# Kernel tuning notes

Measured on AMD Instinct MI355X. Metric: run time of the kernel, lower is better.

Reference implementation:

```python
import jax, jax.numpy as jnp
import numpy as np

B, H, NI, NQ = 4096, 1024, 4096, 2048


def setup_inputs() -> dict:
    key = jax.random.key(0)
    ks = jax.random.split(key, 12)
    state = jax.random.normal(ks[0], (B, H), jnp.float32)
    inputX = jax.random.normal(ks[1], (B, NI), jnp.float32)
    # one-hot next-question vector
    q_idx = jax.random.randint(ks[2], (B,), 0, NQ)
    inputY = jax.nn.one_hot(q_idx, NQ, dtype=jnp.float32)
    truth = jax.random.bernoulli(ks[3], 0.5, (B,)).astype(jnp.float32)
    # torch.nn.Linear default init: U(-1/sqrt(fan_in), 1/sqrt(fan_in)), weight (out,in)
    def lin(kw, kb, out_d, in_d):
        bound = 1.0 / np.sqrt(in_d)
        W = jax.random.uniform(kw, (out_d, in_d), jnp.float32, -bound, bound)
        b = jax.random.uniform(kb, (out_d,), jnp.float32, -bound, bound)
        return W, b
    W_t, b_t = lin(ks[4], ks[5], H, H)    # transfer: n_hidden -> n_hidden
    W_x, b_x = lin(ks[6], ks[7], H, NI)   # linear_x: n_input -> n_hidden
    W_y, b_y = lin(ks[8], ks[9], NQ, H)   # linear_y: n_hidden -> n_questions
    return {"state": state, "inputX": inputX, "inputY": inputY, "truth": truth,
            "W_t": W_t, "b_t": b_t, "W_x": W_x, "b_x": b_x, "W_y": W_y, "b_y": b_y}


def reference(state, inputX, inputY, truth, W_t, b_t, W_x, b_x, W_y, b_y):
    # two small linears + tanh -> new hidden state
    linM = state @ W_t.T + b_t                       # (B, H)
    linX = inputX @ W_x.T + b_x                      # (B, H)
    hidden = jnp.tanh(linM + linX)                   # (B, H)
    # prediction head: linear + sigmoid, mask-select via one-hot sum
    pred_output = jax.nn.sigmoid(hidden @ W_y.T + b_y)  # (B, NQ)
    pred = jnp.sum(pred_output * inputY, axis=1)        # (B,)
    # binary cross entropy, sum reduction; torch clamps log terms at -100
    log_p = jnp.maximum(jnp.log(pred), -100.0)
    log_1mp = jnp.maximum(jnp.log1p(-pred), -100.0)
    err = -jnp.sum(truth * log_p + (1.0 - truth) * log_1mp)
    return (pred, err, hidden)
```

## Files before the change

kernel.cpp:

```cpp
#include <hip/hip_runtime.h>
#include <stdint.h>
#include <math.h>

#define B_DIM 4096
#define H_DIM 1024
#define NI_DIM 4096
#define NQ_DIM 2048
#define K_DIM 5120
#define NKT 160

typedef __attribute__((ext_vector_type(8))) short short8;
typedef __attribute__((ext_vector_type(4))) float f32x4;

__device__ __forceinline__ unsigned short f2bf(float f) {
  unsigned u = __float_as_uint(f);
  u += 0x7FFFu + ((u >> 16) & 1u);
  return (unsigned short)(u >> 16);
}
__device__ __forceinline__ float bf2f(unsigned short s) {
  return __uint_as_float(((unsigned)s) << 16);
}

__device__ __forceinline__ void gload_lds16(const void* g, void* l) {
  __builtin_amdgcn_global_load_lds(
      (__attribute__((address_space(1))) void*)(uintptr_t)g,
      (__attribute__((address_space(3))) void*)l, 16, 0, 0);
}

__global__ __launch_bounds__(256) void cast_all(
    const float* __restrict__ state, const float* __restrict__ inputX,
    const float* __restrict__ Wt, const float* __restrict__ Wx,
    short* __restrict__ Xc, short* __restrict__ Wc) {
  __shared__ __align__(16) short lds[4096];
  const int XTILES = (B_DIM / 128) * NKT;
  int bt = blockIdx.x;
  const float *s0, *s1;
  short* dst;
  if (bt < XTILES) { s0 = state; s1 = inputX; dst = Xc; }
  else { bt -= XTILES; s0 = Wt; s1 = Wx; dst = Wc; }
  const int rowTile = bt / NKT;
  const int kt = bt % NKT;
  const float* src;
  long long srcBase;
  int cols;
  if (kt < 32) { src = s0; cols = 1024; srcBase = (long long)kt * 32; }
  else         { src = s1; cols = 4096; srcBase = (long long)(kt - 32) * 32; }
  const int tid = threadIdx.x;
#pragma unroll
  for (int half = 0; half < 2; ++half) {
    int c = tid + half * 256;
    int r = c >> 2, s = c & 3;
    long long sa = ((long long)(rowTile * 128 + r)) * cols + srcBase + s * 8;
    float4 v0 = *(const float4*)(src + sa);
    float4 v1 = *(const float4*)(src + sa + 4);
    short8 o;
    o[0] = (short)f2bf(v0.x); o[1] = (short)f2bf(v0.y);
    o[2] = (short)f2bf(v0.z); o[3] = (short)f2bf(v0.w);
    o[4] = (short)f2bf(v1.x); o[5] = (short)f2bf(v1.y);
    o[6] = (short)f2bf(v1.z); o[7] = (short)f2bf(v1.w);
    *(short8*)(&lds[(s * 128 + r) * 8]) = o;
  }
  __syncthreads();
  short* dtile = dst + (((long long)rowTile * NKT + kt) * 512) * 8;
#pragma unroll
  for (int half = 0; half < 2; ++half) {
    int c = tid + half * 256;
    *(short8*)(dtile + c * 8) = *(const short8*)(&lds[c * 8]);
  }
}

__device__ __forceinline__ int ep_swz(int col, int rw) {
  int byte = col * 256 + rw * 2;
  byte ^= ((col ^ (col >> 3)) & 7) << 4;
  return byte;
}

__global__ __launch_bounds__(256, 4) void gemm_splitk(
    const short* __restrict__ Xc, const short* __restrict__ Wc,
    short* __restrict__ P, int ntk) {
  __shared__ __align__(16) short SH[16384];
  const int tid = threadIdx.x;
  const int lane = tid & 63;
  const int wid = tid >> 6;
  const int wm = wid >> 1, wn = wid & 1;
  const int fr = lane & 15, fq = lane >> 4;

  const int nwg = gridDim.x;
  const int orig = blockIdx.x;
  const int cpx = nwg >> 3;
  const int swz = (orig & 7) * cpx + (orig >> 3);
  const int bz = swz >> 8;
  const int bm = (swz >> 3) & 31;
  const int bn = swz & 7;
  const int kt0 = bz * ntk;

  const int c0 = tid, c1 = tid + 256;
  const short* gA = Xc + (((long long)bm * NKT + kt0) << 12);
  const short* gB = Wc + (((long long)bn * NKT + kt0) << 12);

  f32x4 acc[4][4] = {};

  gload_lds16(gA + c0 * 8, &SH[c0 * 8]);
  gload_lds16(gA + c1 * 8, &SH[c1 * 8]);
  gload_lds16(gB + c0 * 8, &SH[8192 + c0 * 8]);
  gload_lds16(gB + c1 * 8, &SH[8192 + c1 * 8]);
  __syncthreads();

  int cur = 0;
  for (int t = 0; t < ntk; ++t) {
    if (t + 1 < ntk) {
      const short* nA = gA + (long long)(t + 1) * 4096;
      const short* nB = gB + (long long)(t + 1) * 4096;
      short* lA = &SH[(cur ^ 1) * 4096];
      short* lB = &SH[8192 + (cur ^ 1) * 4096];
      gload_lds16(nA + c0 * 8, lA + c0 * 8);
      gload_lds16(nA + c1 * 8, lA + c1 * 8);
      gload_lds16(nB + c0 * 8, lB + c0 * 8);
      gload_lds16(nB + c1 * 8, lB + c1 * 8);
    }
    const short* a_base = &SH[cur * 4096];
    const short* b_base = &SH[8192 + cur * 4096];
    short8 av[4], bv[4];
#pragma unroll
    for (int i = 0; i < 4; i++) {
      av[i] = *(const short8*)(a_base + (fq * 128 + wm * 64 + i * 16 + fr) * 8);
      bv[i] = *(const short8*)(b_base + (fq * 128 + wn * 64 + i * 16 + fr) * 8);
    }
#pragma unroll
    for (int mi = 0; mi < 4; mi++)
#pragma unroll
      for (int ni = 0; ni < 4; ni++)
        acc[mi][ni] = __builtin_amdgcn_mfma_f32_16x16x32_bf16(
            av[mi], bv[ni], acc[mi][ni], 0, 0, 0);
    __syncthreads();
    cur ^= 1;
  }

#pragma unroll
  for (int ni = 0; ni < 4; ni++) {
    int col = wn * 64 + ni * 16 + fr;
#pragma unroll
    for (int mi = 0; mi < 4; mi++) {
      int rw = wm * 64 + mi * 16 + fq * 4;
      unsigned lo = (unsigned)f2bf(acc[mi][ni][0]) |
                    ((unsigned)f2bf(acc[mi][ni][1]) << 16);
      unsigned hi = (unsigned)f2bf(acc[mi][ni][2]) |
                    ((unsigned)f2bf(acc[mi][ni][3]) << 16);
      uint2 pk; pk.x = lo; pk.y = hi;
      *(uint2*)((char*)SH + ep_swz(col, rw)) = pk;
    }
  }
  __syncthreads();
  short* Pp = P + (long long)bz * B_DIM * H_DIM;
#pragma unroll
  for (int h = 0; h < 8; ++h) {
    int chunk = tid + h * 256;
    int r = chunk >> 4;
    int j = chunk & 15;
    short8 o;
#pragma unroll
    for (int k = 0; k < 8; ++k) {
      o[k] = *(const short*)((char*)SH + ep_swz(j * 8 + k, r));
    }
    *(short8*)(Pp + (long long)(bm * 128 + r) * H_DIM + bn * 128 + j * 8) = o;
  }
}

__global__ __launch_bounds__(256) void fuse_row(
    const short* __restrict__ P, const float* __restrict__ bt,
    const float* __restrict__ bx, const float* __restrict__ Y,
    const float* __restrict__ truth, const float* __restrict__ Wy,
    const float* __restrict__ by, float* __restrict__ predOut,
    float* __restrict__ hidden, float* __restrict__ bce, int S) {
  const int b = blockIdx.x;
  const int tid = threadIdx.x;
  __shared__ int s_cnt;
  __shared__ int s_idx[8];
  __shared__ float s_val[8];
  __shared__ float s_red[4];
  if (tid == 0) s_cnt = 0;

  const int c = tid * 4;
  float s0 = 0.f, s1 = 0.f, s2 = 0.f, s3 = 0.f;
  for (int z = 0; z < S; ++z) {
    const short* Pr = P + ((long long)z * B_DIM + b) * H_DIM + c;
    uint2 u = *(const uint2*)Pr;
    s0 += bf2f((unsigned short)(u.x & 0xffff));
    s1 += bf2f((unsigned short)(u.x >> 16));
    s2 += bf2f((unsigned short)(u.y & 0xffff));
    s3 += bf2f((unsigned short)(u.y >> 16));
  }
  float4 bt4 = *(const float4*)(bt + c);
  float4 bx4 = *(const float4*)(bx + c);
  float h0 = tanhf(s0 + bt4.x + bx4.x);
  float h1 = tanhf(s1 + bt4.y + bx4.y);
  float h2 = tanhf(s2 + bt4.z + bx4.z);
  float h3 = tanhf(s3 + bt4.w + bx4.w);
  float* Hr = hidden + (long long)b * H_DIM + c;
  Hr[0] = h0; Hr[1] = h1; Hr[2] = h2; Hr[3] = h3;

  __syncthreads();
  const float4* Yr = (const float4*)(Y + (long long)b * NQ_DIM);
#pragma unroll
  for (int hh = 0; hh < NQ_DIM / 4 / 256; ++hh) {
    int j = tid + hh * 256;
    float4 v = Yr[j];
    if (v.x != 0.0f) { int p = atomicAdd(&s_cnt, 1); if (p < 8) { s_idx[p] = 4 * j;     s_val[p] = v.x; } }
    if (v.y != 0.0f) { int p = atomicAdd(&s_cnt, 1); if (p < 8) { s_idx[p] = 4 * j + 1; s_val[p] = v.y; } }
    if (v.z != 0.0f) { int p = atomicAdd(&s_cnt, 1); if (p < 8) { s_idx[p] = 4 * j + 2; s_val[p] = v.z; } }
    if (v.w != 0.0f) { int p = atomicAdd(&s_cnt, 1); if (p < 8) { s_idx[p] = 4 * j + 3; s_val[p] = v.w; } }
  }
  __syncthreads();
  int cnt = s_cnt < 8 ? s_cnt : 8;
  float predv = 0.0f;
  for (int it = 0; it < cnt; ++it) {
    int q = s_idx[it];
    float4 w = *(const float4*)(Wy + (long long)q * H_DIM + c);
    float part = h0 * w.x + h1 * w.y + h2 * w.z + h3 * w.w;
#pragma unroll
    for (int off = 32; off > 0; off >>= 1) part += __shfl_down(part, off, 64);
    if ((tid & 63) == 0) s_red[tid >> 6] = part;
    __syncthreads();
    if (tid == 0) {
      float z = s_red[0] + s_red[1] + s_red[2] + s_red[3] + by[q];
      float p = 1.0f / (1.0f + expf(-z));
      predv += s_val[it] * p;
    }
    __syncthreads();
  }
  if (tid == 0) {
    predOut[b] = predv;
    float t = truth[b];
    float lp = fmaxf(logf(predv), -100.0f);
    float l1p = fmaxf(log1pf(-predv), -100.0f);
    bce[b] = -(t * lp + (1.0f - t) * l1p);
  }
}

__global__ __launch_bounds__(256) void reduce_err(
    const float* __restrict__ bce, float* __restrict__ errOut) {
  float s = 0.0f;
  for (int i = threadIdx.x; i < B_DIM; i += 256) s += bce[i];
#pragma unroll
  for (int off = 32; off > 0; off >>= 1) s += __shfl_down(s, off, 64);
  __shared__ float red[4];
  if ((threadIdx.x & 63) == 0) red[threadIdx.x >> 6] = s;
  __syncthreads();
  if (threadIdx.x == 0) errOut[0] = red[0] + red[1] + red[2] + red[3];
}

extern "C" void kernel_launch(void* const* d_in, const int* in_sizes, int n_in,
                              void* d_out, int out_size, void* d_ws, size_t ws_size,
                              hipStream_t stream) {
  (void)in_sizes; (void)n_in; (void)out_size;
  const float* state  = (const float*)d_in[0];
  const float* inputX = (const float*)d_in[1];
  const float* inputY = (const float*)d_in[2];
  const float* truth  = (const float*)d_in[3];
  const float* W_t    = (const float*)d_in[4];
  const float* b_t    = (const float*)d_in[5];
  const float* W_x    = (const float*)d_in[6];
  const float* b_x    = (const float*)d_in[7];
  const float* W_y    = (const float*)d_in[8];
  const float* b_y    = (const float*)d_in[9];

  const size_t XC_B = (size_t)B_DIM * K_DIM * 2;
  const size_t WC_B = (size_t)H_DIM * K_DIM * 2;
  const size_t PART = (size_t)B_DIM * H_DIM * 2;

  int S = 1;
  if (ws_size >= XC_B + WC_B + 4 * PART + 16384) S = 4;
  else if (ws_size >= XC_B + WC_B + 2 * PART + 16384) S = 2;

  short* Xc = (short*)d_ws;
  short* Wc = (short*)((char*)d_ws + XC_B);
  short* P  = (short*)((char*)d_ws + XC_B + WC_B);
  float* bce = (float*)((char*)d_ws + XC_B + WC_B + (size_t)S * PART);

  float* predOut = (float*)d_out;
  float* errOut  = predOut + B_DIM;
  float* hidden  = predOut + B_DIM + 1;

  cast_all<<<(B_DIM / 128 + H_DIM / 128) * NKT, 256, 0, stream>>>(
      state, inputX, W_t, W_x, Xc, Wc);

  gemm_splitk<<<256 * S, 256, 0, stream>>>(Xc, Wc, P, NKT / S);

  fuse_row<<<B_DIM, 256, 0, stream>>>(P, b_t, b_x, inputY, truth, W_y, b_y,
                                      predOut, hidden, bce, S);
  reduce_err<<<1, 256, 0, stream>>>(bce, errOut);
}
```

Baseline: 92.99 us.

## Fuse activation fp32-to-bf16 cast into GEMM A-tile loading

Drops the separate cast pass over state and inputX. The GEMM now loads fp32 activation tiles into registers, packs them to bf16 with v_cvt_pk_bf16_f32 after the MFMA block, and writes them to LDS for the next k-step. Only the weights still go through a standalone cast kernel. This removes a full write-then-read round trip of the bf16 activation matrix through memory, but each GEMM block now reads fp32 A (twice the bytes) and the activation rows are re-read by all 8 column blocks.

```diff
diff --git a/kernel.cpp b/kernel.cpp
--- a/kernel.cpp
+++ b/kernel.cpp
@@ -20,6 +20,11 @@
 __device__ __forceinline__ float bf2f(unsigned short s) {
   return __uint_as_float(((unsigned)s) << 16);
 }
+__device__ __forceinline__ unsigned pkbf(float a, float b) {
+  unsigned r;
+  asm("v_cvt_pk_bf16_f32 %0, %1, %2" : "=v"(r) : "v"(a), "v"(b));
+  return r;
+}
 
 __device__ __forceinline__ void gload_lds16(const void* g, void* l) {
   __builtin_amdgcn_global_load_lds(
@@ -27,24 +32,18 @@
       (__attribute__((address_space(3))) void*)l, 16, 0, 0);
 }
 
-__global__ __launch_bounds__(256) void cast_all(
-    const float* __restrict__ state, const float* __restrict__ inputX,
+__global__ __launch_bounds__(256) void cast_w(
     const float* __restrict__ Wt, const float* __restrict__ Wx,
-    short* __restrict__ Xc, short* __restrict__ Wc) {
+    short* __restrict__ Wc) {
   __shared__ __align__(16) short lds[4096];
-  const int XTILES = (B_DIM / 128) * NKT;
-  int bt = blockIdx.x;
-  const float *s0, *s1;
-  short* dst;
-  if (bt < XTILES) { s0 = state; s1 = inputX; dst = Xc; }
-  else { bt -= XTILES; s0 = Wt; s1 = Wx; dst = Wc; }
+  const int bt = blockIdx.x;
   const int rowTile = bt / NKT;
   const int kt = bt % NKT;
   const float* src;
   long long srcBase;
   int cols;
-  if (kt < 32) { src = s0; cols = 1024; srcBase = (long long)kt * 32; }
-  else         { src = s1; cols = 4096; srcBase = (long long)(kt - 32) * 32; }
+  if (kt < 32) { src = Wt; cols = 1024; srcBase = (long long)kt * 32; }
+  else         { src = Wx; cols = 4096; srcBase = (long long)(kt - 32) * 32; }
   const int tid = threadIdx.x;
 #pragma unroll
   for (int half = 0; half < 2; ++half) {
@@ -61,7 +60,7 @@
     *(short8*)(&lds[(s * 128 + r) * 8]) = o;
   }
   __syncthreads();
-  short* dtile = dst + (((long long)rowTile * NKT + kt) * 512) * 8;
+  short* dtile = Wc + (((long long)rowTile * NKT + kt) * 512) * 8;
 #pragma unroll
   for (int half = 0; half < 2; ++half) {
     int c = tid + half * 256;
@@ -76,8 +75,8 @@
 }
 
 __global__ __launch_bounds__(256, 4) void gemm_splitk(
-    const short* __restrict__ Xc, const short* __restrict__ Wc,
-    short* __restrict__ P, int ntk) {
+    const float* __restrict__ state, const float* __restrict__ inputX,
+    const short* __restrict__ Wc, short* __restrict__ P, int ntk) {
   __shared__ __align__(16) short SH[16384];
   const int tid = threadIdx.x;
   const int lane = tid & 63;
@@ -94,27 +93,46 @@
   const int bn = swz & 7;
   const int kt0 = bz * ntk;
 
+  const int r = tid >> 1, hh = tid & 1;
+  const float* qS = state  + (long long)(bm * 128 + r) * 1024 + hh * 16;
+  const float* qX = inputX + (long long)(bm * 128 + r) * 4096 + hh * 16;
+
   const int c0 = tid, c1 = tid + 256;
-  const short* gA = Xc + (((long long)bm * NKT + kt0) << 12);
   const short* gB = Wc + (((long long)bn * NKT + kt0) << 12);
 
   f32x4 acc[4][4] = {};
-
-  gload_lds16(gA + c0 * 8, &SH[c0 * 8]);
-  gload_lds16(gA + c1 * 8, &SH[c1 * 8]);
-  gload_lds16(gB + c0 * 8, &SH[8192 + c0 * 8]);
-  gload_lds16(gB + c1 * 8, &SH[8192 + c1 * 8]);
+  float4 rA0, rA1, rA2, rA3;
+
+  {
+    int ktg = kt0;
+    const float* q = (ktg < 32) ? (qS + ktg * 32) : (qX + (ktg - 32) * 32);
+    rA0 = *(const float4*)(q);
+    rA1 = *(const float4*)(q + 4);
+    rA2 = *(const float4*)(q + 8);
+    rA3 = *(const float4*)(q + 12);
+    gload_lds16(gB + c0 * 8, &SH[8192 + c0 * 8]);
+    gload_lds16(gB + c1 * 8, &SH[8192 + c1 * 8]);
+    uint4 w0, w1;
+    w0.x = pkbf(rA0.x, rA0.y); w0.y = pkbf(rA0.z, rA0.w);
+    w0.z = pkbf(rA1.x, rA1.y); w0.w = pkbf(rA1.z, rA1.w);
+    w1.x = pkbf(rA2.x, rA2.y); w1.y = pkbf(rA2.z, rA2.w);
+    w1.z = pkbf(rA3.x, rA3.y); w1.w = pkbf(rA3.z, rA3.w);
+    *(uint4*)(&SH[((2 * hh) * 128 + r) * 8]) = w0;
+    *(uint4*)(&SH[((2 * hh + 1) * 128 + r) * 8]) = w1;
+  }
   __syncthreads();
 
   int cur = 0;
   for (int t = 0; t < ntk; ++t) {
     if (t + 1 < ntk) {
-      const short* nA = gA + (long long)(t + 1) * 4096;
+      int ktg = kt0 + t + 1;
+      const float* q = (ktg < 32) ? (qS + ktg * 32) : (qX + (ktg - 32) * 32);
+      rA0 = *(const float4*)(q);
+      rA1 = *(const float4*)(q + 4);
+      rA2 = *(const float4*)(q + 8);
+      rA3 = *(const float4*)(q + 12);
       const short* nB = gB + (long long)(t + 1) * 4096;
-      short* lA = &SH[(cur ^ 1) * 4096];
       short* lB = &SH[8192 + (cur ^ 1) * 4096];
-      gload_lds16(nA + c0 * 8, lA + c0 * 8);
-      gload_lds16(nA + c1 * 8, lA + c1 * 8);
       gload_lds16(nB + c0 * 8, lB + c0 * 8);
       gload_lds16(nB + c1 * 8, lB + c1 * 8);
     }
@@ -132,6 +150,16 @@
       for (int ni = 0; ni < 4; ni++)
         acc[mi][ni] = __builtin_amdgcn_mfma_f32_16x16x32_bf16(
             av[mi], bv[ni], acc[mi][ni], 0, 0, 0);
+    if (t + 1 < ntk) {
+      short* lA = &SH[(cur ^ 1) * 4096];
+      uint4 w0, w1;
+      w0.x = pkbf(rA0.x, rA0.y); w0.y = pkbf(rA0.z, rA0.w);
+      w0.z = pkbf(rA1.x, rA1.y); w0.w = pkbf(rA1.z, rA1.w);
+      w1.x = pkbf(rA2.x, rA2.y); w1.y = pkbf(rA2.z, rA2.w);
+      w1.z = pkbf(rA3.x, rA3.y); w1.w = pkbf(rA3.z, rA3.w);
+      *(uint4*)(lA + ((2 * hh) * 128 + r) * 8) = w0;
+      *(uint4*)(lA + ((2 * hh + 1) * 128 + r) * 8) = w1;
+    }
     __syncthreads();
     cur ^= 1;
   }
@@ -155,14 +183,14 @@
 #pragma unroll
   for (int h = 0; h < 8; ++h) {
     int chunk = tid + h * 256;
-    int r = chunk >> 4;
+    int rr = chunk >> 4;
     int j = chunk & 15;
     short8 o;
 #pragma unroll
     for (int k = 0; k < 8; ++k) {
-      o[k] = *(const short*)((char*)SH + ep_swz(j * 8 + k, r));
-    }
-    *(short8*)(Pp + (long long)(bm * 128 + r) * H_DIM + bn * 128 + j * 8) = o;
+      o[k] = *(const short*)((char*)SH + ep_swz(j * 8 + k, rr));
+    }
+    *(short8*)(Pp + (long long)(bm * 128 + rr) * H_DIM + bn * 128 + j * 8) = o;
   }
 }
 
@@ -264,27 +292,24 @@
   const float* W_y    = (const float*)d_in[8];
   const float* b_y    = (const float*)d_in[9];
 
-  const size_t XC_B = (size_t)B_DIM * K_DIM * 2;
   const size_t WC_B = (size_t)H_DIM * K_DIM * 2;
   const size_t PART = (size_t)B_DIM * H_DIM * 2;
 
   int S = 1;
-  if (ws_size >= XC_B + WC_B + 4 * PART + 16384) S = 4;
-  else if (ws_size >= XC_B + WC_B + 2 * PART + 16384) S = 2;
-
-  short* Xc = (short*)d_ws;
-  short* Wc = (short*)((char*)d_ws + XC_B);
-  short* P  = (short*)((char*)d_ws + XC_B + WC_B);
-  float* bce = (float*)((char*)d_ws + XC_B + WC_B + (size_t)S * PART);
+  if (ws_size >= WC_B + 4 * PART + 16384) S = 4;
+  else if (ws_size >= WC_B + 2 * PART + 16384) S = 2;
+
+  short* Wc = (short*)d_ws;
+  short* P  = (short*)((char*)d_ws + WC_B);
+  float* bce = (float*)((char*)d_ws + WC_B + (size_t)S * PART);
 
   float* predOut = (float*)d_out;
   float* errOut  = predOut + B_DIM;
   float* hidden  = predOut + B_DIM + 1;
 
-  cast_all<<<(B_DIM / 128 + H_DIM / 128) * NKT, 256, 0, stream>>>(
-      state, inputX, W_t, W_x, Xc, Wc);
-
-  gemm_splitk<<<256 * S, 256, 0, stream>>>(Xc, Wc, P, NKT / S);
+  cast_w<<<(H_DIM / 128) * NKT, 256, 0, stream>>>(W_t, W_x, Wc);
+
+  gemm_splitk<<<256 * S, 256, 0, stream>>>(state, inputX, Wc, P, NKT / S);
 
   fuse_row<<<B_DIM, 256, 0, stream>>>(P, b_t, b_x, inputY, truth, W_y, b_y,
                                       predOut, hidden, bce, S);
```

Result: no change. 94.76 us (+1.9%).
